# Performance work log

Measured on AMD Instinct MI355X. Metric: run time of the kernel, lower is better.

The kernel has to match this reference:

```python
import jax, jax.numpy as jnp
import numpy as np

L_LAYERS, D, H, V, S, B = 12, 1024, 16, 50257, 512, 4
DH = D // H
DFF = 4 * D
EPS = 1e-6
STD = 0.02


def setup_inputs() -> dict:
    key = jax.random.key(0)
    ks = jax.random.split(key, 16)
    n = lambda k, shp: (jax.random.normal(k, shp, dtype=jnp.float32) * STD)
    inp = {
        'in_idx': jax.random.randint(ks[0], (B, S), 0, V, dtype=jnp.int32),
        'tok_emb': n(ks[1], (V, D)),          # tied with out_head
        'pos_emb': n(ks[2], (S, D)),
        # per-layer stacked params; Linear stored as [in, out] so y = x @ W
        'Wq': n(ks[3], (L_LAYERS, D, D)),
        'Wk': n(ks[4], (L_LAYERS, D, D)),
        'Wv': n(ks[5], (L_LAYERS, D, D)),
        'Wo': n(ks[6], (L_LAYERS, D, D)),
        'bo': jnp.zeros((L_LAYERS, D), jnp.float32),
        'W1': n(ks[7], (L_LAYERS, D, DFF)),
        'b1': jnp.zeros((L_LAYERS, DFF), jnp.float32),
        'W2': n(ks[8], (L_LAYERS, DFF, D)),
        'b2': jnp.zeros((L_LAYERS, D), jnp.float32),
        'ln1_s': jnp.ones((L_LAYERS, D), jnp.float32),
        'ln1_b': jnp.zeros((L_LAYERS, D), jnp.float32),
        'ln2_s': jnp.ones((L_LAYERS, D), jnp.float32),
        'ln2_b': jnp.zeros((L_LAYERS, D), jnp.float32),
        'lnf_s': jnp.ones((D,), jnp.float32),
        'lnf_b': jnp.zeros((D,), jnp.float32),
    }
    return inp


def _layernorm(x, scale, shift):
    mean = jnp.mean(x, axis=-1, keepdims=True)
    var = jnp.mean(jnp.square(x - mean), axis=-1, keepdims=True)  # unbiased=False
    return scale * (x - mean) / jnp.sqrt(var + EPS) + shift


def _gelu(x):
    c = jnp.sqrt(jnp.asarray(2.0 / jnp.pi, x.dtype))
    return 0.5 * x * (1.0 + jnp.tanh(c * (x + 0.044715 * x * x * x)))


def _gpt_forward(in_idx, tok_emb, pos_emb, Wq, Wk, Wv, Wo, bo, W1, b1, W2, b2,
                 ln1_s, ln1_b, ln2_s, ln2_b, lnf_s, lnf_b):
    b, s = in_idx.shape
    x = tok_emb[in_idx] + pos_emb[:s]  # [B,S,D]
    causal = jnp.triu(jnp.ones((s, s), bool), k=1)  # True above diagonal
    scale = 1.0 / jnp.sqrt(jnp.asarray(DH, x.dtype))
    for i in range(L_LAYERS):
        # --- attention sublayer ---
        h = _layernorm(x, ln1_s[i], ln1_b[i])
        q = (h @ Wq[i]).reshape(b, s, H, DH)
        k = (h @ Wk[i]).reshape(b, s, H, DH)
        v = (h @ Wv[i]).reshape(b, s, H, DH)
        scores = jnp.einsum('bqhd,bkhd->bhqk', q, k)
        scores = jnp.where(causal, -jnp.inf, scores) * scale
        attn = jax.nn.softmax(scores, axis=-1)
        ctx = jnp.einsum('bhqk,bkhd->bqhd', attn, v).reshape(b, s, D)
        x = x + ctx @ Wo[i] + bo[i]
        # --- feed-forward sublayer ---
        h = _layernorm(x, ln2_s[i], ln2_b[i])
        x = x + _gelu(h @ W1[i] + b1[i]) @ W2[i] + b2[i]
    x = _layernorm(x, lnf_s, lnf_b)
    logits = x @ tok_emb.T  # tied out head (no bias)
    return logits


def reference(in_idx, tok_emb, pos_emb, Wq, Wk, Wv, Wo, bo, W1, b1, W2, b2,
              ln1_s, ln1_b, ln2_s, ln2_b, lnf_s, lnf_b):
    return _gpt_forward(in_idx, tok_emb, pos_emb, Wq, Wk, Wv, Wo, bo, W1, b1,
                        W2, b2, ln1_s, ln1_b, ln2_s, ln2_b, lnf_s, lnf_b)
```

## Files before the change

kernel.cpp:

```cpp
#include <hip/hip_runtime.h>


#define LL 12
#define DM 1024
#define NH 16
#define DHD 64
#define NV 50257
#define NVP 50304
#define SQ 512
#define NB 4
#define DF 4096
#define MR (NB * SQ)

typedef short bf16x8 __attribute__((ext_vector_type(8)));
typedef float f32x4 __attribute__((ext_vector_type(4)));
typedef unsigned short u16;

__device__ __forceinline__ u16 f2b(float f) {
  unsigned u = __float_as_uint(f);
  u += 0x7fff + ((u >> 16) & 1);
  return (u16)(u >> 16);
}

__device__ __forceinline__ void gload16(const u16* g, u16* l) {
  __builtin_amdgcn_global_load_lds(
      (const __attribute__((address_space(1))) unsigned*)g,
      (__attribute__((address_space(3))) unsigned*)l, 16, 0, 0);
}

template <int MODE, int TBM, int TBN, int MTLOG>
__global__ __launch_bounds__(256, 2) void gemm_k(
    const u16* __restrict__ A, const u16* __restrict__ B, void* __restrict__ Cp,
    void* __restrict__ Cp2, void* __restrict__ Cp3,
    const float* __restrict__ bias, int N, int K, int lda, int ldb, int ldc) {
  int id = blockIdx.x;
  int q8 = gridDim.x >> 3;
  int swz = (id & 7) * q8 + (id >> 3);
  int mt = swz & ((1 << MTLOG) - 1), nt = swz >> MTLOG;
  int m0 = mt * TBM, n0 = nt * TBN;

  __shared__ u16 As[2][TBM * 64];
  __shared__ u16 Bs[2][TBN * 64];

  int t = threadIdx.x, lane = t & 63, wave = t >> 6;
  int wm = wave >> 1, wn = wave & 1;
  int lr = lane & 15, g = lane >> 4;
  int srow = lane >> 3;
  int sxcol = ((lane & 7) ^ (lane >> 3)) << 3;
  int rsw = (lr & 7) << 3;
  constexpr int FM = TBM / 32, FN = TBN / 32;
  constexpr int CA = TBM / 32, CB = TBN / 32;

  f32x4 acc[FM][FN];
#pragma unroll
  for (int i = 0; i < FM; ++i)
#pragma unroll
    for (int j = 0; j < FN; ++j) acc[i][j] = (f32x4){0.f, 0.f, 0.f, 0.f};

  auto stage = [&](int buf, int kt) {
    int k0 = kt * 64;
#pragma unroll
    for (int v = 0; v < CA; ++v) {
      int c = v * 4 + wave;
      gload16(A + (size_t)(m0 + c * 8 + srow) * lda + k0 + sxcol,
              &As[buf][c * 512]);
    }
#pragma unroll
    for (int v = 0; v < CB; ++v) {
      int c = v * 4 + wave;
      gload16(B + (size_t)(n0 + c * 8 + srow) * ldb + k0 + sxcol,
              &Bs[buf][c * 512]);
    }
  };

  auto compute = [&](int buf) {
    bf16x8 af[FM][2], bq[FN][2];
#pragma unroll
    for (int ks = 0; ks < 2; ++ks) {
      int co = (ks * 32 + g * 8) ^ rsw;
#pragma unroll
      for (int i = 0; i < FM; ++i)
        af[i][ks] = *(const bf16x8*)&As[buf][(wm * (TBM / 2) + i * 16 + lr) * 64 + co];
#pragma unroll
      for (int j = 0; j < FN; ++j)
        bq[j][ks] = *(const bf16x8*)&Bs[buf][(wn * (TBN / 2) + j * 16 + lr) * 64 + co];
    }
#pragma unroll
    for (int ks = 0; ks < 2; ++ks)
#pragma unroll
      for (int i = 0; i < FM; ++i)
#pragma unroll
        for (int j = 0; j < FN; ++j)
          acc[i][j] = __builtin_amdgcn_mfma_f32_16x16x32_bf16(
              af[i][ks], bq[j][ks], acc[i][j], 0, 0, 0);
  };

  int nk = K >> 6;
  stage(0, 0);
  __syncthreads();
  int cur = 0;
  for (int kt = 0; kt < nk - 1; ++kt) {
    stage(cur ^ 1, kt + 1);
    compute(cur);
    __syncthreads();
    cur ^= 1;
  }
  compute(cur);

  int rb = g * 4;
#pragma unroll
  for (int i = 0; i < FM; ++i) {
#pragma unroll
    for (int j = 0; j < FN; ++j) {
      int m = m0 + wm * (TBM / 2) + i * 16 + rb;
      int n = n0 + wn * (TBN / 2) + j * 16 + lr;
      f32x4 a = acc[i][j];
      if constexpr (MODE == 1) {
        float* C = (float*)Cp;
        float bv = bias[n];
#pragma unroll
        for (int r = 0; r < 4; ++r) {
          size_t ix = (size_t)(m + r) * ldc + n;
          C[ix] += a[r] + bv;
        }
      } else if constexpr (MODE == 2) {
        u16* C = (u16*)Cp;
        float bv = bias[n];
#pragma unroll
        for (int r = 0; r < 4; ++r) {
          float u2 = a[r] + bv;
          float gl =
              0.5f * u2 *
              (1.f + tanhf(0.7978845608f * (u2 + 0.044715f * u2 * u2 * u2)));
          C[(size_t)(m + r) * ldc + n] = f2b(gl);
        }
      } else if constexpr (MODE == 6) {
        if (n < NV) {
          float* C = (float*)Cp;
#pragma unroll
          for (int r = 0; r < 4; ++r) C[(size_t)(m + r) * ldc + n] = a[r];
        }
      } else if constexpr (MODE == 7) {
        int sel = n >> 10, nn = n & 1023;
        if (sel < 2) {
          u16* C = sel == 0 ? (u16*)Cp : (u16*)Cp2;
#pragma unroll
          for (int r = 0; r < 4; ++r) C[(size_t)(m + r) * ldc + nn] = f2b(a[r]);
        } else {
          u16* C = (u16*)Cp3;
          int bb = m >> 9, s2 = m & (SQ - 1);
          ushort4 w4;
          w4.x = f2b(a[0]); w4.y = f2b(a[1]);
          w4.z = f2b(a[2]); w4.w = f2b(a[3]);
          *(ushort4*)&C[((size_t)bb * DM + nn) * SQ + s2] = w4;
        }
      }
    }
  }
}

__global__ __launch_bounds__(256) void fattn_k(const u16* __restrict__ qb,
                                               const u16* __restrict__ kb,
                                               const u16* __restrict__ vt,
                                               u16* __restrict__ cx) {
  int id = blockIdx.x;
  int qt = id >> 6, bh = id & 63;
  int b = bh >> 4, hh = bh & 15;
  int t = threadIdx.x, lane = t & 63, w = t >> 6;
  int lr = lane & 15, g = lane >> 4;

  __shared__ u16 Kt[64 * 72];
  __shared__ u16 Vt[64 * 72];
  __shared__ u16 Pl[4 * 16 * 72];

  int qw = qt * 64 + w * 16;

  bf16x8 aQ[2];
#pragma unroll
  for (int f = 0; f < 2; ++f)
    aQ[f] = *(const bf16x8*)&qb[(size_t)(b * SQ + qw + lr) * DM + hh * DHD +
                                f * 32 + g * 8];

  f32x4 o[4];
#pragma unroll
  for (int j = 0; j < 4; ++j) o[j] = (f32x4){0.f, 0.f, 0.f, 0.f};
  f32x4 m4 = (f32x4){-3e38f, -3e38f, -3e38f, -3e38f};
  f32x4 l4 = (f32x4){0.f, 0.f, 0.f, 0.f};
  u16* Pw = &Pl[w * 16 * 72];

  for (int kt = 0; kt <= qt; ++kt) {
    int k0 = kt * 64;
#pragma unroll
    for (int it = 0; it < 2; ++it) {
      int c = t + it * 256;
      int row = c >> 3, ch = c & 7;
      int4 kv = *(const int4*)&kb[(size_t)(b * SQ + k0 + row) * DM + hh * DHD +
                                  ch * 8];
      int4 vv = *(const int4*)&vt[(size_t)(b * DM + hh * DHD + row) * SQ + k0 +
                                  ch * 8];
      *(int4*)&Kt[row * 72 + ch * 8] = kv;
      *(int4*)&Vt[row * 72 + ch * 8] = vv;
    }
    __syncthreads();

    f32x4 s[4];
#pragma unroll
    for (int j = 0; j < 4; ++j) s[j] = (f32x4){0.f, 0.f, 0.f, 0.f};
#pragma unroll
    for (int j = 0; j < 4; ++j)
#pragma unroll
      for (int f = 0; f < 2; ++f) {
        bf16x8 bk = *(const bf16x8*)&Kt[(j * 16 + lr) * 72 + f * 32 + g * 8];
        s[j] =
            __builtin_amdgcn_mfma_f32_16x16x32_bf16(aQ[f], bk, s[j], 0, 0, 0);
      }
#pragma unroll
    for (int j = 0; j < 4; ++j) {
      int kcol = k0 + j * 16 + lr;
#pragma unroll
      for (int r = 0; r < 4; ++r) {
        float sv = s[j][r] * 0.125f;
        if (kt == qt && kcol > qw + g * 4 + r) sv = -1e30f;
        s[j][r] = sv;
      }
    }
    f32x4 fr;
#pragma unroll
    for (int r = 0; r < 4; ++r) {
      float v = fmaxf(fmaxf(s[0][r], s[1][r]), fmaxf(s[2][r], s[3][r]));
#pragma unroll
      for (int d = 1; d < 16; d <<= 1) v = fmaxf(v, __shfl_xor(v, d));
      float mn = fmaxf(m4[r], v);
      fr[r] = __expf(m4[r] - mn);
      m4[r] = mn;
    }
#pragma unroll
    for (int j = 0; j < 4; ++j)
#pragma unroll
      for (int r = 0; r < 4; ++r) o[j][r] *= fr[r];
    f32x4 ps = (f32x4){0.f, 0.f, 0.f, 0.f};
#pragma unroll
    for (int j = 0; j < 4; ++j)
#pragma unroll
      for (int r = 0; r < 4; ++r) {
        float p = __expf(s[j][r] - m4[r]);
        s[j][r] = p;
        ps[r] += p;
      }
#pragma unroll
    for (int r = 0; r < 4; ++r) {
      float v = ps[r];
#pragma unroll
      for (int d = 1; d < 16; d <<= 1) v += __shfl_xor(v, d);
      l4[r] = l4[r] * fr[r] + v;
    }
#pragma unroll
    for (int j = 0; j < 4; ++j)
#pragma unroll
      for (int r = 0; r < 4; ++r)
        Pw[(g * 4 + r) * 72 + j * 16 + lr] = f2b(s[j][r]);
#pragma unroll
    for (int f = 0; f < 2; ++f) {
      bf16x8 ap = *(const bf16x8*)&Pw[lr * 72 + f * 32 + g * 8];
#pragma unroll
      for (int j = 0; j < 4; ++j) {
        bf16x8 bv = *(const bf16x8*)&Vt[(j * 16 + lr) * 72 + f * 32 + g * 8];
        o[j] = __builtin_amdgcn_mfma_f32_16x16x32_bf16(ap, bv, o[j], 0, 0, 0);
      }
    }
    __syncthreads();
  }

#pragma unroll
  for (int r = 0; r < 4; ++r) {
    float inv = 1.f / l4[r];
#pragma unroll
    for (int j = 0; j < 4; ++j)
      cx[(size_t)(b * SQ + qw + g * 4 + r) * DM + hh * DHD + j * 16 + lr] =
          f2b(o[j][r] * inv);
  }
}

__global__ __launch_bounds__(256) void transpln_k(
    const float* __restrict__ Wq, const float* __restrict__ Wk,
    const float* __restrict__ Wv, const float* __restrict__ Wo,
    const float* __restrict__ W1, const float* __restrict__ W2,
    u16* __restrict__ wb, const float* __restrict__ x,
    const float* __restrict__ sc, const float* __restrict__ sh,
    u16* __restrict__ o) {
  __shared__ u16 tl[64][72];
  __shared__ float red[8];
  int t = threadIdx.x;
  if (blockIdx.x < 3072) {
    int id = blockIdx.x;
    const float* src;
    u16* dst;
    int K, N, ktile, ntile;
    if (id < 1024) {
      int mat = id >> 8, rem = id & 255;
      ntile = rem & 15; ktile = rem >> 4;
      src = mat == 0 ? Wq : mat == 1 ? Wk : mat == 2 ? Wv : Wo;
      dst = wb + (size_t)mat * DM * DM;
      K = DM; N = DM;
    } else if (id < 2048) {
      int rem = id - 1024;
      ntile = rem & 63; ktile = rem >> 6;
      src = W1; dst = wb + (size_t)4 * DM * DM;
      K = DM; N = DF;
    } else {
      int rem = id - 2048;
      ntile = rem & 15; ktile = rem >> 4;
      src = W2; dst = wb + (size_t)4 * DM * DM + (size_t)DM * DF;
      K = DF; N = DM;
    }
    int n0 = ntile * 64, k0 = ktile * 64;
    int tn = (t & 15) * 4, tk = t >> 4;
#pragma unroll
    for (int it = 0; it < 4; ++it) {
      int k = tk + it * 16;
      float4 v = *(const float4*)(src + (size_t)(k0 + k) * N + n0 + tn);
      tl[tn + 0][k] = f2b(v.x);
      tl[tn + 1][k] = f2b(v.y);
      tl[tn + 2][k] = f2b(v.z);
      tl[tn + 3][k] = f2b(v.w);
    }
    __syncthreads();
    int wn = t >> 3, wk = (t & 7) * 8;
#pragma unroll
    for (int it = 0; it < 2; ++it) {
      int n = wn + it * 32;
      int4 v = *(const int4*)&tl[n][wk];
      *(int4*)(dst + (size_t)(n0 + n) * K + k0 + wk) = v;
    }
  } else {
    int row = blockIdx.x - 3072;
    const float* xr = x + (size_t)row * DM;
    float4 v = *(const float4*)(xr + t * 4);
    float s = v.x + v.y + v.z + v.w;
#pragma unroll
    for (int d = 32; d; d >>= 1) s += __shfl_xor(s, d);
    if ((t & 63) == 0) red[t >> 6] = s;
    __syncthreads();
    float mean = (red[0] + red[1] + red[2] + red[3]) * (1.f / DM);
    float dx = v.x - mean, dy = v.y - mean, dz = v.z - mean, dw = v.w - mean;
    float s2 = dx * dx + dy * dy + dz * dz + dw * dw;
#pragma unroll
    for (int d = 32; d; d >>= 1) s2 += __shfl_xor(s2, d);
    if ((t & 63) == 0) red[4 + (t >> 6)] = s2;
    __syncthreads();
    float var = (red[4] + red[5] + red[6] + red[7]) * (1.f / DM);
    float rstd = 1.f / sqrtf(var + 1e-6f);
    float4 gg = *(const float4*)(sc + t * 4);
    float4 b = *(const float4*)(sh + t * 4);
    ushort4 w4;
    w4.x = f2b(gg.x * (dx * rstd) + b.x);
    w4.y = f2b(gg.y * (dy * rstd) + b.y);
    w4.z = f2b(gg.z * (dz * rstd) + b.z);
    w4.w = f2b(gg.w * (dw * rstd) + b.w);
    *(ushort4*)(o + (size_t)row * DM + t * 4) = w4;
  }
}

__global__ __launch_bounds__(256) void ln_k(const float* __restrict__ x,
                                            const float* __restrict__ sc,
                                            const float* __restrict__ sh,
                                            u16* __restrict__ o) {
  int row = blockIdx.x, t = threadIdx.x;
  const float* xr = x + (size_t)row * DM;
  float4 v = *(const float4*)(xr + t * 4);
  float s = v.x + v.y + v.z + v.w;
#pragma unroll
  for (int d = 32; d; d >>= 1) s += __shfl_xor(s, d);
  __shared__ float red[8];
  if ((t & 63) == 0) red[t >> 6] = s;
  __syncthreads();
  float mean = (red[0] + red[1] + red[2] + red[3]) * (1.f / DM);
  float dx = v.x - mean, dy = v.y - mean, dz = v.z - mean, dw = v.w - mean;
  float s2 = dx * dx + dy * dy + dz * dz + dw * dw;
#pragma unroll
  for (int d = 32; d; d >>= 1) s2 += __shfl_xor(s2, d);
  if ((t & 63) == 0) red[4 + (t >> 6)] = s2;
  __syncthreads();
  float var = (red[4] + red[5] + red[6] + red[7]) * (1.f / DM);
  float rstd = 1.f / sqrtf(var + 1e-6f);
  float4 g = *(const float4*)(sc + t * 4);
  float4 b = *(const float4*)(sh + t * 4);
  ushort4 w4;
  w4.x = f2b(g.x * (dx * rstd) + b.x);
  w4.y = f2b(g.y * (dy * rstd) + b.y);
  w4.z = f2b(g.z * (dz * rstd) + b.z);
  w4.w = f2b(g.w * (dw * rstd) + b.w);
  *(ushort4*)(o + (size_t)row * DM + t * 4) = w4;
}

__global__ __launch_bounds__(256) void embtok_k(const int* __restrict__ idx,
                                                const float* __restrict__ tok,
                                                const float* __restrict__ pos,
                                                float* __restrict__ x,
                                                u16* __restrict__ tokT) {
  int t = threadIdx.x;
  if (blockIdx.x < MR) {
    int row = blockIdx.x;
    int s = row & (SQ - 1);
    int id = idx[row];
    float4 a = *(const float4*)(tok + (size_t)id * DM + t * 4);
    float4 p = *(const float4*)(pos + (size_t)s * DM + t * 4);
    a.x += p.x; a.y += p.y; a.z += p.z; a.w += p.w;
    *(float4*)(x + (size_t)row * DM + t * 4) = a;
  } else {
    size_t r = blockIdx.x - MR;
    ushort4 w = {0, 0, 0, 0};
    if (r < NV) {
      float4 v = *(const float4*)(tok + r * DM + t * 4);
      w.x = f2b(v.x); w.y = f2b(v.y); w.z = f2b(v.z); w.w = f2b(v.w);
    }
    *(ushort4*)(tokT + r * DM + t * 4) = w;
  }
}

extern "C" void kernel_launch(void* const* d_in, const int* in_sizes, int n_in,
                              void* d_out, int out_size, void* d_ws,
                              size_t ws_size, hipStream_t stream) {
  const int* idx = (const int*)d_in[0];
  const float* tok = (const float*)d_in[1];
  const float* pos = (const float*)d_in[2];
  const float* Wq = (const float*)d_in[3];
  const float* Wk = (const float*)d_in[4];
  const float* Wv = (const float*)d_in[5];
  const float* Wo = (const float*)d_in[6];
  const float* bo = (const float*)d_in[7];
  const float* W1 = (const float*)d_in[8];
  const float* b1 = (const float*)d_in[9];
  const float* W2 = (const float*)d_in[10];
  const float* b2 = (const float*)d_in[11];
  const float* ln1s = (const float*)d_in[12];
  const float* ln1b = (const float*)d_in[13];
  const float* ln2s = (const float*)d_in[14];
  const float* ln2b = (const float*)d_in[15];
  const float* lnfs = (const float*)d_in[16];
  const float* lnfb = (const float*)d_in[17];
  float* out = (float*)d_out;

  char* w = (char*)d_ws;
  float* x = (float*)w;  w += (size_t)MR * DM * 4;
  u16* h = (u16*)w;      w += (size_t)MR * DM * 2;
  u16* qb = (u16*)w;     w += (size_t)MR * DM * 2;
  u16* kb = (u16*)w;     w += (size_t)MR * DM * 2;
  u16* vt = (u16*)w;     w += (size_t)NB * DM * SQ * 2;
  u16* ff = (u16*)w;     w += (size_t)MR * DF * 2;
  u16* wb = (u16*)w;     w += ((size_t)4 * DM * DM + 2 * (size_t)DM * DF) * 2;
  u16* tokT = (u16*)w;
  u16* cx = h;
  u16* wo_b = wb + (size_t)3 * DM * DM;
  u16* wb1 = wb + (size_t)4 * DM * DM;
  u16* wb2 = wb1 + (size_t)DM * DF;

  dim3 T(256);
  embtok_k<<<MR + NVP, T, 0, stream>>>(idx, tok, pos, x, tokT);
  for (int l = 0; l < LL; ++l) {
    size_t wo_ = (size_t)l * DM * DM;
    size_t w1_ = (size_t)l * DM * DF;
    transpln_k<<<5120, T, 0, stream>>>(Wq + wo_, Wk + wo_, Wv + wo_, Wo + wo_,
                                       W1 + w1_, W2 + w1_, wb, x, ln1s + l * DM,
                                       ln1b + l * DM, h);
    gemm_k<7, 64, 128, 5><<<768, T, 0, stream>>>(
        h, wb, qb, kb, vt, nullptr, 3 * DM, DM, DM, DM, DM);
    fattn_k<<<512, T, 0, stream>>>(qb, kb, vt, cx);
    gemm_k<1, 64, 64, 5><<<512, T, 0, stream>>>(
        cx, wo_b, x, nullptr, nullptr, bo + l * DM, DM, DM, DM, DM, DM);
    ln_k<<<MR, T, 0, stream>>>(x, ln2s + l * DM, ln2b + l * DM, h);
    gemm_k<2, 128, 128, 4><<<512, T, 0, stream>>>(
        h, wb1, ff, nullptr, nullptr, b1 + l * DF, DF, DM, DM, DM, DF);
    gemm_k<1, 64, 64, 5><<<512, T, 0, stream>>>(
        ff, wb2, x, nullptr, nullptr, b2 + l * DM, DM, DF, DF, DF, DM);
  }
  ln_k<<<MR, T, 0, stream>>>(x, lnfs, lnfb, h);
  gemm_k<6, 128, 128, 4><<<6288, T, 0, stream>>>(
      h, tokT, out, nullptr, nullptr, nullptr, NV, DM, DM, DM, NV);
}
```

Baseline: 2.285 ms.

## Add triple-buffered GEMM pipeline with vmcnt waits and larger LM-head tiles

Generalizes the GEMM kernel over thread count and buffer depth. It moves the layer GEMMs to a 3-stage LDS pipeline that uses explicit vmcnt waits instead of a full sync on every k-step, and interleaves MFMAs with B-fragment loads under s_setprio. The FFN1 GEMM switches to 64x128 tiles, and the LM-head GEMM uses 256x256 tiles with 512 threads and 8 waves, padding the vocab to 50432. This is meant to hide global-load latency and raise MFMA utilization, at the cost of more LDS per block and possible occupancy or register pressure.

```diff
diff --git a/kernel.cpp b/kernel.cpp
--- a/kernel.cpp
+++ b/kernel.cpp
@@ -6,7 +6,7 @@
 #define NH 16
 #define DHD 64
 #define NV 50257
-#define NVP 50304
+#define NVP 50432
 #define SQ 512
 #define NB 4
 #define DF 4096
@@ -28,28 +28,47 @@
       (__attribute__((address_space(3))) unsigned*)l, 16, 0, 0);
 }
 
-template <int MODE, int TBM, int TBN, int MTLOG>
-__global__ __launch_bounds__(256, 2) void gemm_k(
+template <int N>
+__device__ __forceinline__ void waitvm() {
+  if constexpr (N == 0) asm volatile("s_waitcnt vmcnt(0)" ::: "memory");
+  else if constexpr (N == 4) asm volatile("s_waitcnt vmcnt(4)" ::: "memory");
+  else if constexpr (N == 6) asm volatile("s_waitcnt vmcnt(6)" ::: "memory");
+  else if constexpr (N == 8) asm volatile("s_waitcnt vmcnt(8)" ::: "memory");
+  else if constexpr (N == 12) asm volatile("s_waitcnt vmcnt(12)" ::: "memory");
+  else asm volatile("s_waitcnt vmcnt(16)" ::: "memory");
+}
+
+__device__ __forceinline__ void barrier_sb() {
+  __builtin_amdgcn_s_barrier();
+  __builtin_amdgcn_sched_barrier(0);
+}
+
+template <int MODE, int TBM, int TBN, int MTLOG, int NT, int NBUF>
+__global__ __launch_bounds__(NT, 2) void gemm_k(
     const u16* __restrict__ A, const u16* __restrict__ B, void* __restrict__ Cp,
     void* __restrict__ Cp2, void* __restrict__ Cp3,
     const float* __restrict__ bias, int N, int K, int lda, int ldb, int ldc) {
+  constexpr int NW = NT / 64;
+  constexpr int WN = (NW == 8) ? 4 : 2, WM = 2;
+  constexpr int FM = TBM / (WM * 16), FN = TBN / (WN * 16);
+  constexpr int LPT = (TBM + TBN) / (8 * NW);
+  constexpr int NCA = TBM / 8;
+
   int id = blockIdx.x;
   int q8 = gridDim.x >> 3;
   int swz = (id & 7) * q8 + (id >> 3);
   int mt = swz & ((1 << MTLOG) - 1), nt = swz >> MTLOG;
   int m0 = mt * TBM, n0 = nt * TBN;
 
-  __shared__ u16 As[2][TBM * 64];
-  __shared__ u16 Bs[2][TBN * 64];
+  __shared__ u16 As[NBUF][TBM * 64];
+  __shared__ u16 Bs[NBUF][TBN * 64];
 
   int t = threadIdx.x, lane = t & 63, wave = t >> 6;
-  int wm = wave >> 1, wn = wave & 1;
+  int wm = wave / WN, wn = wave % WN;
   int lr = lane & 15, g = lane >> 4;
   int srow = lane >> 3;
   int sxcol = ((lane & 7) ^ (lane >> 3)) << 3;
   int rsw = (lr & 7) << 3;
-  constexpr int FM = TBM / 32, FN = TBN / 32;
-  constexpr int CA = TBM / 32, CB = TBN / 32;
 
   f32x4 acc[FM][FN];
 #pragma unroll
@@ -57,63 +76,84 @@
 #pragma unroll
     for (int j = 0; j < FN; ++j) acc[i][j] = (f32x4){0.f, 0.f, 0.f, 0.f};
 
-  auto stage = [&](int buf, int kt) {
-    int k0 = kt * 64;
-#pragma unroll
-    for (int v = 0; v < CA; ++v) {
-      int c = v * 4 + wave;
-      gload16(A + (size_t)(m0 + c * 8 + srow) * lda + k0 + sxcol,
-              &As[buf][c * 512]);
-    }
-#pragma unroll
-    for (int v = 0; v < CB; ++v) {
-      int c = v * 4 + wave;
-      gload16(B + (size_t)(n0 + c * 8 + srow) * ldb + k0 + sxcol,
-              &Bs[buf][c * 512]);
+  auto stage = [&](int buf, int ktile) {
+    int k0 = ktile * 64;
+#pragma unroll
+    for (int v = 0; v < LPT; ++v) {
+      int c = v * NW + wave;
+      if (c < NCA) {
+        gload16(A + (size_t)(m0 + c * 8 + srow) * lda + k0 + sxcol,
+                &As[buf][c * 512]);
+      } else {
+        int cb = c - NCA;
+        gload16(B + (size_t)(n0 + cb * 8 + srow) * ldb + k0 + sxcol,
+                &Bs[buf][cb * 512]);
+      }
     }
   };
 
   auto compute = [&](int buf) {
-    bf16x8 af[FM][2], bq[FN][2];
 #pragma unroll
     for (int ks = 0; ks < 2; ++ks) {
       int co = (ks * 32 + g * 8) ^ rsw;
+      bf16x8 af[FM];
 #pragma unroll
       for (int i = 0; i < FM; ++i)
-        af[i][ks] = *(const bf16x8*)&As[buf][(wm * (TBM / 2) + i * 16 + lr) * 64 + co];
-#pragma unroll
-      for (int j = 0; j < FN; ++j)
-        bq[j][ks] = *(const bf16x8*)&Bs[buf][(wn * (TBN / 2) + j * 16 + lr) * 64 + co];
-    }
-#pragma unroll
-    for (int ks = 0; ks < 2; ++ks)
-#pragma unroll
-      for (int i = 0; i < FM; ++i)
-#pragma unroll
-        for (int j = 0; j < FN; ++j)
-          acc[i][j] = __builtin_amdgcn_mfma_f32_16x16x32_bf16(
-              af[i][ks], bq[j][ks], acc[i][j], 0, 0, 0);
+        af[i] =
+            *(const bf16x8*)&As[buf][(wm * (TBM / WM) + i * 16 + lr) * 64 + co];
+#pragma unroll
+      for (int jh = 0; jh < FN; jh += 2) {
+        bf16x8 b0 =
+            *(const bf16x8*)&Bs[buf][(wn * (TBN / WN) + jh * 16 + lr) * 64 + co];
+        bf16x8 b1 = *(const bf16x8*)&Bs[buf][(wn * (TBN / WN) + (jh + 1) * 16 + lr) *
+                                                 64 + co];
+        __builtin_amdgcn_s_setprio(1);
+#pragma unroll
+        for (int i = 0; i < FM; ++i)
+          acc[i][jh] =
+              __builtin_amdgcn_mfma_f32_16x16x32_bf16(af[i], b0, acc[i][jh], 0, 0, 0);
+#pragma unroll
+        for (int i = 0; i < FM; ++i)
+          acc[i][jh + 1] = __builtin_amdgcn_mfma_f32_16x16x32_bf16(
+              af[i], b1, acc[i][jh + 1], 0, 0, 0);
+        __builtin_amdgcn_s_setprio(0);
+      }
+    }
   };
 
   int nk = K >> 6;
-  stage(0, 0);
-  __syncthreads();
-  int cur = 0;
-  for (int kt = 0; kt < nk - 1; ++kt) {
-    stage(cur ^ 1, kt + 1);
-    compute(cur);
-    __syncthreads();
-    cur ^= 1;
-  }
-  compute(cur);
+#pragma unroll
+  for (int p = 0; p < NBUF - 1; ++p) stage(p, p);
+  int cbuf = 0, sbuf = NBUF - 1;
+  int kt = 0;
+#pragma unroll 1
+  for (; kt < nk - (NBUF - 1); ++kt) {
+    stage(sbuf, kt + NBUF - 1);
+    waitvm<(NBUF - 1) * LPT>();
+    barrier_sb();
+    compute(cbuf);
+    barrier_sb();
+    cbuf = cbuf + 1 == NBUF ? 0 : cbuf + 1;
+    sbuf = sbuf + 1 == NBUF ? 0 : sbuf + 1;
+  }
+  if constexpr (NBUF == 3) {
+    waitvm<LPT>();
+    barrier_sb();
+    compute(cbuf);
+    barrier_sb();
+    cbuf = cbuf + 1 == NBUF ? 0 : cbuf + 1;
+  }
+  waitvm<0>();
+  barrier_sb();
+  compute(cbuf);
 
   int rb = g * 4;
 #pragma unroll
   for (int i = 0; i < FM; ++i) {
 #pragma unroll
     for (int j = 0; j < FN; ++j) {
-      int m = m0 + wm * (TBM / 2) + i * 16 + rb;
-      int n = n0 + wn * (TBN / 2) + j * 16 + lr;
+      int m = m0 + wm * (TBM / WM) + i * 16 + rb;
+      int n = n0 + wn * (TBN / WN) + j * 16 + lr;
       f32x4 a = acc[i][j];
       if constexpr (MODE == 1) {
         float* C = (float*)Cp;
@@ -463,18 +503,18 @@
     transpln_k<<<5120, T, 0, stream>>>(Wq + wo_, Wk + wo_, Wv + wo_, Wo + wo_,
                                        W1 + w1_, W2 + w1_, wb, x, ln1s + l * DM,
                                        ln1b + l * DM, h);
-    gemm_k<7, 64, 128, 5><<<768, T, 0, stream>>>(
+    gemm_k<7, 64, 128, 5, 256, 3><<<768, T, 0, stream>>>(
         h, wb, qb, kb, vt, nullptr, 3 * DM, DM, DM, DM, DM);
     fattn_k<<<512, T, 0, stream>>>(qb, kb, vt, cx);
-    gemm_k<1, 64, 64, 5><<<512, T, 0, stream>>>(
+    gemm_k<1, 64, 64, 5, 256, 3><<<512, T, 0, stream>>>(
         cx, wo_b, x, nullptr, nullptr, bo + l * DM, DM, DM, DM, DM, DM);
     ln_k<<<MR, T, 0, stream>>>(x, ln2s + l * DM, ln2b + l * DM, h);
-    gemm_k<2, 128, 128, 4><<<512, T, 0, stream>>>(
+    gemm_k<2, 64, 128, 5, 256, 3><<<1024, T, 0, stream>>>(
         h, wb1, ff, nullptr, nullptr, b1 + l * DF, DF, DM, DM, DM, DF);
-    gemm_k<1, 64, 64, 5><<<512, T, 0, stream>>>(
+    gemm_k<1, 64, 64, 5, 256, 3><<<512, T, 0, stream>>>(
         ff, wb2, x, nullptr, nullptr, b2 + l * DM, DM, DF, DF, DF, DM);
   }
   ln_k<<<MR, T, 0, stream>>>(x, lnfs, lnfb, h);
-  gemm_k<6, 128, 128, 4><<<6288, T, 0, stream>>>(
+  gemm_k<6, 256, 256, 3, 512, 2><<<1576, dim3(512), 0, stream>>>(
       h, tokT, out, nullptr, nullptr, nullptr, NV, DM, DM, DM, NV);
 }
```

Measured after the change: 2.513 ms. +10.0%, slower.

## Add dedicated 256x256-tile LM-head GEMM kernel with 512 threads

Applied to the files above, without the earlier changes.

Replaces the generic 128x128 tiled GEMM for the vocabulary projection with a specialized kernel using 256x256 tiles, 8 waves, XOR-swizzled LDS staging, a grid swizzle for L2 locality, and s_setprio around MFMA bursts. The vocab padding is raised so it divides evenly into 256-wide tiles. The larger tiles raise arithmetic intensity and cut global reloads of the activation and embedding matrices. The cost is heavy LDS (128KB double-buffered) and register pressure, which limits occupancy, plus extra wasted columns in the padded tail.

```diff
diff --git a/kernel.cpp b/kernel.cpp
--- a/kernel.cpp
+++ b/kernel.cpp
@@ -6,7 +6,7 @@
 #define NH 16
 #define DHD 64
 #define NV 50257
-#define NVP 50304
+#define NVP 50432
 #define SQ 512
 #define NB 4
 #define DF 4096
@@ -80,10 +80,12 @@
       int co = (ks * 32 + g * 8) ^ rsw;
 #pragma unroll
       for (int i = 0; i < FM; ++i)
-        af[i][ks] = *(const bf16x8*)&As[buf][(wm * (TBM / 2) + i * 16 + lr) * 64 + co];
+        af[i][ks] =
+            *(const bf16x8*)&As[buf][(wm * (TBM / 2) + i * 16 + lr) * 64 + co];
 #pragma unroll
       for (int j = 0; j < FN; ++j)
-        bq[j][ks] = *(const bf16x8*)&Bs[buf][(wn * (TBN / 2) + j * 16 + lr) * 64 + co];
+        bq[j][ks] =
+            *(const bf16x8*)&Bs[buf][(wn * (TBN / 2) + j * 16 + lr) * 64 + co];
     }
 #pragma unroll
     for (int ks = 0; ks < 2; ++ks)
@@ -134,12 +136,6 @@
               (1.f + tanhf(0.7978845608f * (u2 + 0.044715f * u2 * u2 * u2)));
           C[(size_t)(m + r) * ldc + n] = f2b(gl);
         }
-      } else if constexpr (MODE == 6) {
-        if (n < NV) {
-          float* C = (float*)Cp;
-#pragma unroll
-          for (int r = 0; r < 4; ++r) C[(size_t)(m + r) * ldc + n] = a[r];
-        }
       } else if constexpr (MODE == 7) {
         int sel = n >> 10, nn = n & 1023;
         if (sel < 2) {
@@ -154,6 +150,105 @@
           w4.z = f2b(a[2]); w4.w = f2b(a[3]);
           *(ushort4*)&C[((size_t)bb * DM + nn) * SQ + s2] = w4;
         }
+      }
+    }
+  }
+}
+
+__global__ __launch_bounds__(512, 2) void gemmL_k(const u16* __restrict__ A,
+                                                  const u16* __restrict__ B,
+                                                  float* __restrict__ C) {
+  int id = blockIdx.x;
+  int q8 = gridDim.x >> 3;
+  int swz = (id & 7) * q8 + (id >> 3);
+  int mt = swz & 7, nt = swz >> 3;
+  int m0 = mt * 256, n0 = nt * 256;
+
+  __shared__ u16 As[2][256 * 64];
+  __shared__ u16 Bs[2][256 * 64];
+
+  int t = threadIdx.x, lane = t & 63, wave = t >> 6;
+  int wm = wave >> 2, wn = wave & 3;
+  int lr = lane & 15, g = lane >> 4;
+  int rsw = (lr & 7) << 3;
+
+  f32x4 acc[8][4];
+#pragma unroll
+  for (int i = 0; i < 8; ++i)
+#pragma unroll
+    for (int j = 0; j < 4; ++j) acc[i][j] = (f32x4){0.f, 0.f, 0.f, 0.f};
+
+  auto stage = [&](int slot, int kt) {
+    int k0 = kt * 64;
+#pragma unroll
+    for (int v = 0; v < 4; ++v) {
+      int c = v * 512 + t;
+      int row = c >> 3, cc = c & 7;
+      gload16(A + (size_t)(m0 + row) * DM + k0 + ((cc ^ (row & 7)) << 3),
+              &As[slot][c * 8]);
+    }
+#pragma unroll
+    for (int v = 0; v < 4; ++v) {
+      int c = v * 512 + t;
+      int row = c >> 3, cc = c & 7;
+      gload16(B + (size_t)(n0 + row) * DM + k0 + ((cc ^ (row & 7)) << 3),
+              &Bs[slot][c * 8]);
+    }
+  };
+
+  auto phase = [&](int slot, int ks) {
+    int co = (ks * 32 + g * 8) ^ rsw;
+    bf16x8 af[8], bq[4];
+#pragma unroll
+    for (int i = 0; i < 8; ++i)
+      af[i] = *(const bf16x8*)&As[slot][(wm * 128 + i * 16 + lr) * 64 + co];
+#pragma unroll
+    for (int j = 0; j < 4; ++j)
+      bq[j] = *(const bf16x8*)&Bs[slot][(wn * 64 + j * 16 + lr) * 64 + co];
+    __builtin_amdgcn_s_setprio(1);
+#pragma unroll
+    for (int i = 0; i < 8; ++i)
+#pragma unroll
+      for (int j = 0; j < 4; ++j)
+        acc[i][j] = __builtin_amdgcn_mfma_f32_16x16x32_bf16(af[i], bq[j],
+                                                            acc[i][j], 0, 0, 0);
+    __builtin_amdgcn_s_setprio(0);
+  };
+
+  constexpr int NIT = DM / 128;
+  stage(0, 0);
+  stage(1, 1);
+#pragma unroll 1
+  for (int it = 0; it < NIT; ++it) {
+    asm volatile("s_waitcnt vmcnt(8)" ::: "memory");
+    __builtin_amdgcn_s_barrier();
+    phase(0, 0);
+    phase(0, 1);
+    __builtin_amdgcn_s_barrier();
+    if (it + 1 < NIT) {
+      stage(0, 2 * it + 2);
+      asm volatile("s_waitcnt vmcnt(8)" ::: "memory");
+    } else {
+      asm volatile("s_waitcnt vmcnt(0)" ::: "memory");
+    }
+    __builtin_amdgcn_s_barrier();
+    phase(1, 0);
+    phase(1, 1);
+    __builtin_amdgcn_s_barrier();
+    if (it + 1 < NIT) stage(1, 2 * it + 3);
+  }
+
+  int rb = g * 4;
+#pragma unroll
+  for (int i = 0; i < 8; ++i) {
+#pragma unroll
+    for (int j = 0; j < 4; ++j) {
+      int m = m0 + wm * 128 + i * 16 + rb;
+      int n = n0 + wn * 64 + j * 16 + lr;
+      if (n < NV) {
+        f32x4 a = acc[i][j];
+#pragma unroll
+        for (int r = 0; r < 4; ++r) C[(size_t)(m + r) * NV + n] = a[r];
       }
     }
   }
@@ -475,6 +570,5 @@
         ff, wb2, x, nullptr, nullptr, b2 + l * DM, DM, DF, DF, DF, DM);
   }
   ln_k<<<MR, T, 0, stream>>>(x, lnfs, lnfb, h);
-  gemm_k<6, 128, 128, 4><<<6288, T, 0, stream>>>(
-      h, tokT, out, nullptr, nullptr, nullptr, NV, DM, DM, DM, NV);
-}
+  gemmL_k<<<1576, dim3(512), 0, stream>>>(h, tokT, out);
+}
```

After: 2.435 ms. 6.6% more time.
